# Performance work log

Measured on AMD Instinct MI355X. Metric: run time of the kernel, lower is better.

Reference implementation:

```python
import jax, jax.numpy as jnp
import numpy as np
import math

BATCH = 32
F_IN, F_OUT = 16, 32
B_IN, B_OUT = 16, 8
N_SPEC = B_OUT * (4 * B_OUT ** 2 - 1) // 3  # sum_{l<b_out} (2l+1)^2 = 680
ALPHAS = [2.0 * np.pi * a / 6.0 for a in range(6)]
GAMMAS = [2.0 * np.pi * c / 4.0 for c in range(4)]
GRID = [(al, np.pi / 16.0, ga) for al in ALPHAS for ga in GAMMAS]  # 24 (alpha, beta, gamma) points
SCALING = 1.0 / math.sqrt(len(GRID) * F_IN * B_OUT ** 3 / B_IN ** 3)


def _wigner_d(l, beta):
    """Wigner small-d matrix d^l_{m'm}(beta), centered order m',m=-l..l, quantum/Condon-Shortley."""
    lg = math.lgamma
    cb, sb = math.cos(beta / 2.0), math.sin(beta / 2.0)
    d = np.zeros((2 * l + 1, 2 * l + 1))
    for i, mp in enumerate(range(-l, l + 1)):
        for j, m in enumerate(range(-l, l + 1)):
            pref = 0.5 * (lg(l + mp + 1) + lg(l - mp + 1) + lg(l + m + 1) + lg(l - m + 1))
            tot = 0.0
            for s in range(max(0, m - mp), min(l + m, l - mp) + 1):
                den = lg(l + m - s + 1) + lg(s + 1) + lg(mp - m + s + 1) + lg(l - mp - s + 1)
                tot += ((-1.0) ** (mp - m + s) * math.exp(pref - den)
                        * cb ** (2 * l + m - mp - 2 * s) * sb ** (mp - m + 2 * s))
            d[i, j] = tot
    return d


def _quad_weights(b):
    """SOFT quadrature weights at beta_j = pi(2j+1)/(4b); 1/(2b)^2 absorbs the unnormalized 2D FFT."""
    k = np.arange(b)
    j = np.arange(2 * b)
    w = (2.0 / b) * np.sin(np.pi * (2 * j + 1) / (4.0 * b)) * (
        np.sin(np.pi * np.outer(2 * j + 1, 2 * k + 1) / (4.0 * b)) / (2 * k + 1)).sum(axis=1)
    return w / (2 * b) ** 2


def _setup_tables():
    betas_in = np.pi * (2 * np.arange(2 * B_IN) + 1) / (4.0 * B_IN)
    betas_out = np.pi * (2 * np.arange(2 * B_OUT) + 1) / (4.0 * B_OUT)
    w = _quad_weights(B_IN)
    wig_fwd = np.stack([np.concatenate([w[j] * _wigner_d(l, b).ravel() for l in range(B_OUT)])
                        for j, b in enumerate(betas_in)])          # [2*B_IN, N_SPEC]
    wig_inv = np.stack([np.concatenate([(2 * l + 1) * _wigner_d(l, b).ravel() for l in range(B_OUT)])
                        for b in betas_out])                       # [2*B_OUT, N_SPEC]
    F = np.zeros((len(GRID), N_SPEC), dtype=np.complex128)
    for p, (al, be, ga) in enumerate(GRID):
        blocks = []
        for l in range(B_OUT):
            m = np.arange(-l, l + 1)
            D = np.exp(-1j * m[:, None] * al) * _wigner_d(l, be) * np.exp(-1j * m[None, :] * ga)
            blocks.append(np.conj(D).ravel())
        F[p] = np.concatenate(blocks)
    return (wig_fwd.astype(np.float32), wig_inv.astype(np.float32),
            F.real.astype(np.float32), F.imag.astype(np.float32))


def _freq_idx(l, n):
    # packed frequencies -l..-1,0..l with wraparound into an FFT axis of length n
    return np.r_[np.arange(n - l, n), np.arange(l + 1)] if l > 0 else np.arange(1)


def _forward(x, kernel, bias, wigner_fwd, wigner_inv, ft_re, ft_im):
    xf = jnp.fft.fft2(x)  # FFT over (alpha, gamma): [B, Fin, 2b_in, 2b_in, 2b_in] complex64
    # SO3_fft_real: weighted Wigner-d contraction over beta, per degree l
    xhat = []
    for l in range(B_OUT):
        idx = _freq_idx(l, 2 * B_IN)
        xx = xf[:, :, :, idx[:, None], idx[None, :]]  # [B, Fin, beta, 2l+1, 2l+1]
        s0 = l * (4 * l * l - 1) // 3
        wl = wigner_fwd[:, s0:s0 + (2 * l + 1) ** 2].reshape(2 * B_IN, 2 * l + 1, 2 * l + 1)
        xhat.append(jnp.einsum('bmn,zfbmn->mnzf', wl, xx))  # [2l+1, 2l+1, B, Fin]
    # so3_rft of the scaled kernel on the grid: yhat [N_SPEC, Fin, Fout]
    Fc = ft_re + 1j * ft_im  # [P, N_SPEC]
    yhat = jnp.einsum('iop,ps->sio', (kernel * SCALING).astype(jnp.complex64), Fc)
    # so3_mm: per-degree z^l = x^l (y^l)^H, then inverse SO3 FFT
    B = x.shape[0]
    ff = jnp.zeros((B, F_OUT, 2 * B_OUT, 2 * B_OUT, 2 * B_OUT), dtype=xf.dtype)
    for l in range(B_OUT):
        s0 = l * (4 * l * l - 1) // 3
        yl = yhat[s0:s0 + (2 * l + 1) ** 2].reshape(2 * l + 1, 2 * l + 1, F_IN, F_OUT)
        zl = jnp.einsum('mkzf,nkfg->mnzg', xhat[l], jnp.conj(yl))  # [2l+1, 2l+1, B, Fout]
        wl = wigner_inv[:, s0:s0 + (2 * l + 1) ** 2].reshape(2 * B_OUT, 2 * l + 1, 2 * l + 1)
        o = jnp.einsum('mnzg,bmn->zgbmn', zl, wl)  # [B, Fout, beta_out, 2l+1, 2l+1]
        idx = _freq_idx(l, 2 * B_OUT)
        ff = ff.at[:, :, :, idx[:, None], idx[None, :]].add(o)
    out = jnp.real(jnp.fft.ifft2(ff)) * float((2 * B_OUT) ** 2)  # undo ifft 1/N^2, keep real part
    return out + bias


def setup_inputs():
    key = jax.random.key(0)
    k1, k2 = jax.random.split(key)
    x = jax.random.normal(k1, (BATCH, F_IN, 2 * B_IN, 2 * B_IN, 2 * B_IN), dtype=jnp.float32)
    kernel = jax.random.uniform(k2, (F_IN, F_OUT, len(GRID)), minval=-1.0, maxval=1.0, dtype=jnp.float32)
    bias = jnp.zeros((1, F_OUT, 1, 1, 1), jnp.float32)
    wf, wi, fre, fim = _setup_tables()
    return {"x": x, "kernel": kernel, "bias": bias,
            "wigner_fwd": jnp.asarray(wf), "wigner_inv": jnp.asarray(wi),
            "ft_re": jnp.asarray(fre), "ft_im": jnp.asarray(fim)}


def reference(x, kernel, bias, wigner_fwd, wigner_inv, ft_re, ft_im):
    return _forward(x, kernel, bias, wigner_fwd, wigner_inv, ft_re, ft_im)
```

## Files before the change

### kernel.cpp

```cpp
#include <hip/hip_runtime.h>
#include <math.h>


#define NS 680
#define NR 372
#define NP 24
#define NW 15
#define SLB 4
#define SCALING 0.14433756729740643f

__device__ __constant__ int c_s0[9] = {0, 1, 10, 35, 84, 165, 286, 455, 680};
__device__ __constant__ int c_o[9]  = {0, 1, 7, 22, 50, 95, 161, 252, 372};

__device__ __constant__ float2 TW32[32] = {
    { 1.0000000000f,  0.0000000000f}, { 0.9807852804f, -0.1950903220f},
    { 0.9238795325f, -0.3826834324f}, { 0.8314696123f, -0.5555702330f},
    { 0.7071067812f, -0.7071067812f}, { 0.5555702330f, -0.8314696123f},
    { 0.3826834324f, -0.9238795325f}, { 0.1950903220f, -0.9807852804f},
    { 0.0000000000f, -1.0000000000f}, {-0.1950903220f, -0.9807852804f},
    {-0.3826834324f, -0.9238795325f}, {-0.5555702330f, -0.8314696123f},
    {-0.7071067812f, -0.7071067812f}, {-0.8314696123f, -0.5555702330f},
    {-0.9238795325f, -0.3826834324f}, {-0.9807852804f, -0.1950903220f},
    {-1.0000000000f,  0.0000000000f}, {-0.9807852804f,  0.1950903220f},
    {-0.9238795325f,  0.3826834324f}, {-0.8314696123f,  0.5555702330f},
    {-0.7071067812f,  0.7071067812f}, {-0.5555702330f,  0.8314696123f},
    {-0.3826834324f,  0.9238795325f}, {-0.1950903220f,  0.9807852804f},
    { 0.0000000000f,  1.0000000000f}, { 0.1950903220f,  0.9807852804f},
    { 0.3826834324f,  0.9238795325f}, { 0.5555702330f,  0.8314696123f},
    { 0.7071067812f,  0.7071067812f}, { 0.8314696123f,  0.5555702330f},
    { 0.9238795325f,  0.3826834324f}, { 0.9807852804f,  0.1950903220f}};

__device__ __constant__ float2 TW16P[16] = {
    { 1.0000000000f,  0.0000000000f}, { 0.9238795325f,  0.3826834324f},
    { 0.7071067812f,  0.7071067812f}, { 0.3826834324f,  0.9238795325f},
    { 0.0000000000f,  1.0000000000f}, {-0.3826834324f,  0.9238795325f},
    {-0.7071067812f,  0.7071067812f}, {-0.9238795325f,  0.3826834324f},
    {-1.0000000000f,  0.0000000000f}, {-0.9238795325f, -0.3826834324f},
    {-0.7071067812f, -0.7071067812f}, {-0.3826834324f, -0.9238795325f},
    { 0.0000000000f, -1.0000000000f}, { 0.3826834324f, -0.9238795325f},
    { 0.7071067812f, -0.7071067812f}, { 0.9238795325f, -0.3826834324f}};

__global__ __launch_bounds__(256) void A12(const float* __restrict__ x,
                                           float2* __restrict__ xf2) {
    __shared__ __align__(16) float  sx[SLB * 1152];
    __shared__ __align__(16) float2 st[SLB][8][34];
    __shared__ float2 tw[32];
    int blk = blockIdx.x;
    int tid = threadIdx.x;
    if (tid < 32) tw[tid] = TW32[tid];
    {
        const float4* xs = (const float4*)(x + (size_t)blk * (SLB * 1024));
#pragma unroll
        for (int q = 0; q < SLB; q++) {
            int idx = q * 256 + tid;
            float4 v4 = xs[idx];
            int sl = idx >> 8, w = idx & 255;
            *(float4*)&sx[sl * 1152 + (w >> 3) * 36 + (w & 7) * 4] = v4;
        }
    }
    __syncthreads();
    {
        int u = tid >> 3, n = tid & 7;
        float sgn = (n & 1) ? -1.f : 1.f;
        float2 t8[8];
#pragma unroll
        for (int c = 0; c < 8; c++) t8[c] = tw[(n * c) & 31];
        float2 fa1 = tw[(8 * n) & 31];
#pragma unroll
        for (int sl = 0; sl < SLB; sl++) {
            const float* row = &sx[sl * 1152 + u * 36];
            float4 x0 = *(float4*)&row[0],  x1 = *(float4*)&row[4];
            float4 x2 = *(float4*)&row[8],  x3 = *(float4*)&row[12];
            float4 x4 = *(float4*)&row[16], x5 = *(float4*)&row[20];
            float4 x6 = *(float4*)&row[24], x7 = *(float4*)&row[28];
            float y0  = fmaf(sgn, x4.x, x0.x), y1  = fmaf(sgn, x4.y, x0.y);
            float y2  = fmaf(sgn, x4.z, x0.z), y3  = fmaf(sgn, x4.w, x0.w);
            float y4  = fmaf(sgn, x5.x, x1.x), y5  = fmaf(sgn, x5.y, x1.y);
            float y6  = fmaf(sgn, x5.z, x1.z), y7  = fmaf(sgn, x5.w, x1.w);
            float y8  = fmaf(sgn, x6.x, x2.x), y9  = fmaf(sgn, x6.y, x2.y);
            float y10 = fmaf(sgn, x6.z, x2.z), y11 = fmaf(sgn, x6.w, x2.w);
            float y12 = fmaf(sgn, x7.x, x3.x), y13 = fmaf(sgn, x7.y, x3.y);
            float y14 = fmaf(sgn, x7.z, x3.z), y15 = fmaf(sgn, x7.w, x3.w);
            float p0r = y0 * t8[0].x + y1 * t8[1].x + y2 * t8[2].x + y3 * t8[3].x
                      + y4 * t8[4].x + y5 * t8[5].x + y6 * t8[6].x + y7 * t8[7].x;
            float p0i = y0 * t8[0].y + y1 * t8[1].y + y2 * t8[2].y + y3 * t8[3].y
                      + y4 * t8[4].y + y5 * t8[5].y + y6 * t8[6].y + y7 * t8[7].y;
            float p1r = y8 * t8[0].x + y9 * t8[1].x + y10 * t8[2].x + y11 * t8[3].x
                      + y12 * t8[4].x + y13 * t8[5].x + y14 * t8[6].x + y15 * t8[7].x;
            float p1i = y8 * t8[0].y + y9 * t8[1].y + y10 * t8[2].y + y11 * t8[3].y
                      + y12 * t8[4].y + y13 * t8[5].y + y14 * t8[6].y + y15 * t8[7].y;
            float re = p0r + fa1.x * p1r - fa1.y * p1i;
            float im = p0i + fa1.x * p1i + fa1.y * p1r;
            st[sl][n][u] = make_float2(re, im);
        }
    }
    __syncthreads();
    {
        int sl = tid >> 6, m = (tid >> 3) & 7, jj = tid & 7;
        float2 t8[8], fa[4];
#pragma unroll
        for (int c = 0; c < 8; c++) t8[c] = tw[(m * c) & 31];
        fa[0] = make_float2(1.f, 0.f);
#pragma unroll
        for (int a = 1; a < 4; a++) fa[a] = tw[(8 * m * a) & 31];
        float reP = 0.f, imP = 0.f, reN = 0.f, imN = 0.f;
#pragma unroll
        for (int a = 0; a < 4; a++) {
            const float4* spt = (const float4*)&st[sl][jj][a * 8];
            float4 r0 = spt[0], r1 = spt[1], r2 = spt[2], r3 = spt[3];
            float A = r0.x * t8[0].x + r0.z * t8[1].x + r1.x * t8[2].x + r1.z * t8[3].x
                    + r2.x * t8[4].x + r2.z * t8[5].x + r3.x * t8[6].x + r3.z * t8[7].x;
            float B = r0.y * t8[0].y + r0.w * t8[1].y + r1.y * t8[2].y + r1.w * t8[3].y
                    + r2.y * t8[4].y + r2.w * t8[5].y + r3.y * t8[6].y + r3.w * t8[7].y;
            float C = r0.x * t8[0].y + r0.z * t8[1].y + r1.x * t8[2].y + r1.z * t8[3].y
                    + r2.x * t8[4].y + r2.z * t8[5].y + r3.x * t8[6].y + r3.z * t8[7].y;
            float D = r0.y * t8[0].x + r0.w * t8[1].x + r1.y * t8[2].x + r1.w * t8[3].x
                    + r2.y * t8[4].x + r2.w * t8[5].x + r3.y * t8[6].x + r3.w * t8[7].x;
            float prP = A - B, piP = C + D;
            float prN = A + B, piN = C - D;
            reP += fa[a].x * prP - fa[a].y * piP;
            imP += fa[a].x * piP + fa[a].y * prP;
            reN += fa[a].x * prN - fa[a].y * piN;
            imN += fa[a].x * piN + fa[a].y * prN;
        }
        int slice = blk * SLB + sl;
        float2* ob = xf2 + (size_t)slice * 120 + m * 15;
        ob[7 + jj] = make_float2(reP, imP);
        if (jj) ob[7 - jj] = make_float2(reN, imN);
    }
}

__global__ void kP(const float* __restrict__ kern, const float* __restrict__ fre,
                   const float* __restrict__ fim, const float* __restrict__ wf,
                   const float* __restrict__ wi, float2* __restrict__ yhat,
                   float* __restrict__ wfT, float* __restrict__ wiTd) {
    int idx = blockIdx.x * blockDim.x + threadIdx.x;
    if (idx < NS * 512) {
        int s = idx >> 9, fg = idx & 511;
        float re = 0.f, im = 0.f;
        for (int p = 0; p < NP; p++) {
            float kv = kern[fg * NP + p];
            re += kv * fre[p * NS + s];
            im += kv * fim[p * NS + s];
        }
        yhat[(size_t)s * 512 + fg] = make_float2(re * SCALING, im * SCALING);
        return;
    }
    int j = idx - NS * 512;
    if (j < NR * 32) {
        int sp = j >> 5, b = j & 31;
        int l = 0;
#pragma unroll
        for (int t = 1; t < 8; t++) if (sp >= c_o[t]) l = t;
        int K = 2 * l + 1, r = sp - c_o[l];
        int m = r / K, jn = r - m * K;
        int sf = c_s0[l] + (m + l) * K + jn;
        wfT[sp * 32 + b] = wf[b * NS + sf];
        return;
    }
    int k = j - NR * 32;
    if (k >= 16384) return;
    int ni = k & 15, mm = (k >> 4) & 7, b8 = (k >> 7) & 7;
    int l = (k >> 10) & 7, bh = k >> 13;
    int nn = ni - 7;
    float v = 0.f;
    if (ni < 15 && mm <= l && nn >= -l && nn <= l) {
        int K = 2 * l + 1;
        v = wi[(bh * 8 + b8) * NS + c_s0[l] + (mm + l) * K + (nn + l)];
    }
    wiTd[k] = v;
}

__global__ __launch_bounds__(256) void A3(const float2* __restrict__ xf2,
                                          const float* __restrict__ wfT,
                                          float2* __restrict__ xhat) {
    __shared__ float2 sxf[32 * 120];
    int zf = blockIdx.x >> 1, sh = blockIdx.x & 1;
    int tid = threadIdx.x;
    for (int t = tid; t < 32 * 120; t += 256)
        sxf[t] = xf2[(size_t)zf * (32 * 120) + t];
    __syncthreads();
    if (tid < 186) {
        int sp = sh * 186 + tid;
        int l = 0;
#pragma unroll
        for (int t = 1; t < 8; t++) if (sp >= c_o[t]) l = t;
        int K = 2 * l + 1, r = sp - c_o[l];
        int m = r / K, jn = r - m * K;
        int cell = m * 15 + (jn - l + 7);
        const float4* wp = (const float4*)(wfT + sp * 32);
        const float2* xp = sxf + cell;
        float re = 0.f, im = 0.f;
#pragma unroll
        for (int q = 0; q < 8; q++) {
            float4 w4 = wp[q];
            float2 v0 = xp[(q * 4 + 0) * 120];
            float2 v1 = xp[(q * 4 + 1) * 120];
            float2 v2 = xp[(q * 4 + 2) * 120];
            float2 v3 = xp[(q * 4 + 3) * 120];
            re += w4.x * v0.x + w4.y * v1.x + w4.z * v2.x + w4.w * v3.x;
            im += w4.x * v0.y + w4.y * v1.y + w4.z * v2.y + w4.w * v3.y;
        }
        xhat[(size_t)sp * 512 + zf] = make_float2(re, im);
    }
}

__global__ __launch_bounds__(256) void kD(const float2* __restrict__ xhat,
                                          const float2* __restrict__ yhat,
                                          float2* __restrict__ zbuf) {
    __shared__ float2 Xs[4][16][18];
    __shared__ float2 Ys[4][16][34];
    int sp = 371 - (blockIdx.x >> 1);
    int zh = blockIdx.x & 1;
    int l = 0;
#pragma unroll
    for (int t = 1; t < 8; t++) if (sp >= c_o[t]) l = t;
    int K = 2 * l + 1, r = sp - c_o[l];
    int m = r / K, jn = r - m * K;
    int sX0 = c_o[l] + m * K;
    int sY0 = c_s0[l] + jn * K;
    int tid = threadIdx.x;
    int zl = tid >> 4;
    int g0 = (tid & 15) * 2;
    float2 acc0 = make_float2(0.f, 0.f), acc1 = make_float2(0.f, 0.f);
    int nchunks = (K + 3) >> 2;
    for (int chunk = 0; chunk < nchunks; ++chunk) {
#pragma unroll
        for (int kw = 0; kw < 4; kw++) {
            int k = chunk * 4 + kw;
            if (k < K)
                Xs[kw][tid & 15][tid >> 4] =
                    xhat[(size_t)(sX0 + k) * 512 + (zh * 16 + (tid >> 4)) * 16 + (tid & 15)];
        }
#pragma unroll
        for (int it = 0; it < 8; it++) {
            int kw = it >> 1;
            int fg = (it & 1) * 256 + tid;
            int k = chunk * 4 + kw;
            if (k < K)
                Ys[kw][fg >> 5][fg & 31] = yhat[(size_t)(sY0 + k) * 512 + fg];
        }
        __syncthreads();
#pragma unroll
        for (int kw = 0; kw < 4; kw++) {
            int k = chunk * 4 + kw;
            if (k < K) {
#pragma unroll
                for (int f = 0; f < 16; f++) {
                    float2 xv  = Xs[kw][f][zl];
                    float2 yv0 = Ys[kw][f][g0];
                    float2 yv1 = Ys[kw][f][g0 + 1];
                    acc0.x += xv.x * yv0.x + xv.y * yv0.y;
                    acc0.y += xv.y * yv0.x - xv.x * yv0.y;
                    acc1.x += xv.x * yv1.x + xv.y * yv1.y;
                    acc1.y += xv.y * yv1.x - xv.x * yv1.y;
                }
            }
        }
        __syncthreads();
    }
    int z0 = zh * 16 + zl;
    zbuf[(size_t)sp * 1024 + z0 * 32 + g0]     = acc0;
    zbuf[(size_t)sp * 1024 + z0 * 32 + g0 + 1] = acc1;
}

__global__ __launch_bounds__(256) void kE3(const float2* __restrict__ zbuf,
                                           const float* __restrict__ wiTd,
                                           const float* __restrict__ bias,
                                           float* __restrict__ out) {
    __shared__ float2 szp[384];
    __shared__ float2 g1[8][129];
    __shared__ float2 tw[16];
    int zg = blockIdx.x >> 1, bh = blockIdx.x & 1;
    int g = zg & 31;
    int tid = threadIdx.x;
    if (tid < 16) tw[tid] = TW16P[tid];
    if (tid < 8)   szp[tid] = make_float2(0.f, 0.f);
    if (tid >= 252) szp[tid + 128] = make_float2(0.f, 0.f);
    for (int t = tid; t < NR; t += 256) szp[8 + t] = zbuf[(size_t)t * 1024 + zg];
    __syncthreads();
    if (tid < 128) {
        int b8 = tid & 7, mm = (tid >> 3) & 7, vh = tid >> 6;
        const int co[8] = {0, 1, 7, 22, 50, 95, 161, 252};
        float2 ff[15];
#pragma unroll
        for (int n = 0; n < 15; n++) ff[n] = make_float2(0.f, 0.f);
#pragma unroll
        for (int l = 0; l < 8; l++) {
            const float4* wl = (const float4*)(wiTd + ((((bh * 8 + l) * 8 + b8) * 8 + mm) << 4));
            float4 w0 = wl[0], w1 = wl[1], w2 = wl[2], w3 = wl[3];
            float wreg[16] = {w0.x, w0.y, w0.z, w0.w, w1.x, w1.y, w1.z, w1.w,
                              w2.x, w2.y, w2.z, w2.w, w3.x, w3.y, w3.z, w3.w};
            int sp = 1 + co[l] + mm * (2 * l + 1) + l;
#pragma unroll
            for (int ni = 0; ni < 15; ni++) {
                float w = wreg[ni];
                float2 v = szp[sp + ni];
                ff[ni].x += w * v.x; ff[ni].y += w * v.y;
            }
        }
#pragma unroll
        for (int j = 0; j < 8; j++) {
            int v = vh * 8 + j;
            float re = 0.f, im = 0.f;
#pragma unroll
            for (int n = 0; n < 15; n++) {
                float2 c = tw[((n - 7) * v) & 15];
                float2 a = ff[n];
                re += a.x * c.x - a.y * c.y;
                im += a.x * c.y + a.y * c.x;
            }
            g1[b8][mm * 16 + v] = make_float2(re, im);
        }
    }
    __syncthreads();
    {
        int b8 = tid & 7, u = (tid >> 3) & 15, vh = tid >> 7;
        int b = bh * 8 + b8;
        int v0 = vh * 8;
        float o[8];
#pragma unroll
        for (int j = 0; j < 8; j++) o[j] = g1[b8][v0 + j].x;
#pragma unroll
        for (int m = 1; m < 8; m++) {
            float2 c = tw[(m * u) & 15];
#pragma unroll
            for (int j = 0; j < 8; j++) {
                float2 a = g1[b8][m * 16 + v0 + j];
                o[j] += 2.f * (a.x * c.x - a.y * c.y);
            }
        }
        float bv = bias[g];
        float* ob = out + ((size_t)zg * 16 + b) * 256 + u * 16 + v0;
        *(float4*)&ob[0] = make_float4(o[0] + bv, o[1] + bv, o[2] + bv, o[3] + bv);
        *(float4*)&ob[4] = make_float4(o[4] + bv, o[5] + bv, o[6] + bv, o[7] + bv);
    }
}

extern "C" void kernel_launch(void* const* d_in, const int* in_sizes, int n_in,
                              void* d_out, int out_size, void* d_ws, size_t ws_size,
                              hipStream_t stream) {
    const float* x    = (const float*)d_in[0];
    const float* kern = (const float*)d_in[1];
    const float* bias = (const float*)d_in[2];
    const float* wf   = (const float*)d_in[3];
    const float* wi   = (const float*)d_in[4];
    const float* fre  = (const float*)d_in[5];
    const float* fim  = (const float*)d_in[6];
    float* out = (float*)d_out;

    char* ws = (char*)d_ws;
    float2* xf2  = (float2*)ws;
    float2* xhat = (float2*)(ws + 15728640);
    float2* yhat = (float2*)(ws + 17252352);
    float2* zbuf = (float2*)(ws + 20037632);
    float*  wfT  = (float*)(ws + 23085056);
    float*  wiTd = (float*)(ws + 23132672);

    A12<<<4096, 256, 0, stream>>>(x, xf2);
    kP<<<1471, 256, 0, stream>>>(kern, fre, fim, wf, wi, yhat, wfT, wiTd);
    A3<<<1024, 256, 0, stream>>>(xf2, wfT, xhat);
    kD<<<744, 256, 0, stream>>>(xhat, yhat, zbuf);
    kE3<<<2048, 256, 0, stream>>>(zbuf, wiTd, bias, out);
}
```

Before: 92.66 us.

## Transpose zbuf via new kernel for coalesced kE3 loads; pad g1 shared array

Adds a tiled shared-memory transpose kernel that rewrites zbuf from [sp][zg] to [zg][sp] layout. kE3 can then read its 372 spectral coefficients contiguously instead of with a 1024-element stride. The g1 shared buffer is also re-padded (stride 17 per m, 139 per b8) to reduce bank conflicts. The cost is an extra kernel launch plus roughly 6 MB of extra global traffic through the transpose.

```diff
diff --git a/kernel.cpp b/kernel.cpp
--- a/kernel.cpp
+++ b/kernel.cpp
@@ -264,12 +264,33 @@
     zbuf[(size_t)sp * 1024 + z0 * 32 + g0 + 1] = acc1;
 }
 
-__global__ __launch_bounds__(256) void kE3(const float2* __restrict__ zbuf,
+__global__ __launch_bounds__(256) void kX(const float2* __restrict__ zbuf,
+                                          float2* __restrict__ zbufT) {
+    __shared__ float2 st[32][33];
+    int spT = blockIdx.x % 12, zgT = blockIdx.x / 12;
+    int sp0 = spT * 32, zg0 = zgT * 32;
+    int tid = threadIdx.x;
+#pragma unroll
+    for (int r = 0; r < 4; r++) {
+        int idx = r * 256 + tid;
+        int i = idx >> 5, j = idx & 31;
+        if (sp0 + i < NR) st[i][j] = zbuf[(size_t)(sp0 + i) * 1024 + zg0 + j];
+    }
+    __syncthreads();
+#pragma unroll
+    for (int r = 0; r < 4; r++) {
+        int idx = r * 256 + tid;
+        int i = idx >> 5, j = idx & 31;
+        if (sp0 + j < NR) zbufT[(size_t)(zg0 + i) * NR + sp0 + j] = st[j][i];
+    }
+}
+
+__global__ __launch_bounds__(256) void kE3(const float2* __restrict__ zbufT,
                                            const float* __restrict__ wiTd,
                                            const float* __restrict__ bias,
                                            float* __restrict__ out) {
     __shared__ float2 szp[384];
-    __shared__ float2 g1[8][129];
+    __shared__ float2 g1[8 * 139];
     __shared__ float2 tw[16];
     int zg = blockIdx.x >> 1, bh = blockIdx.x & 1;
     int g = zg & 31;
@@ -277,7 +298,7 @@
     if (tid < 16) tw[tid] = TW16P[tid];
     if (tid < 8)   szp[tid] = make_float2(0.f, 0.f);
     if (tid >= 252) szp[tid + 128] = make_float2(0.f, 0.f);
-    for (int t = tid; t < NR; t += 256) szp[8 + t] = zbuf[(size_t)t * 1024 + zg];
+    for (int t = tid; t < NR; t += 256) szp[8 + t] = zbufT[(size_t)zg * NR + t];
     __syncthreads();
     if (tid < 128) {
         int b8 = tid & 7, mm = (tid >> 3) & 7, vh = tid >> 6;
@@ -310,7 +331,7 @@
                 re += a.x * c.x - a.y * c.y;
                 im += a.x * c.y + a.y * c.x;
             }
-            g1[b8][mm * 16 + v] = make_float2(re, im);
+            g1[b8 * 139 + mm * 17 + v] = make_float2(re, im);
         }
     }
     __syncthreads();
@@ -320,13 +341,13 @@
         int v0 = vh * 8;
         float o[8];
 #pragma unroll
-        for (int j = 0; j < 8; j++) o[j] = g1[b8][v0 + j].x;
+        for (int j = 0; j < 8; j++) o[j] = g1[b8 * 139 + v0 + j].x;
 #pragma unroll
         for (int m = 1; m < 8; m++) {
             float2 c = tw[(m * u) & 15];
 #pragma unroll
             for (int j = 0; j < 8; j++) {
-                float2 a = g1[b8][m * 16 + v0 + j];
+                float2 a = g1[b8 * 139 + m * 17 + v0 + j];
                 o[j] += 2.f * (a.x * c.x - a.y * c.y);
             }
         }
@@ -350,16 +371,18 @@
     float* out = (float*)d_out;
 
     char* ws = (char*)d_ws;
-    float2* xf2  = (float2*)ws;
-    float2* xhat = (float2*)(ws + 15728640);
-    float2* yhat = (float2*)(ws + 17252352);
-    float2* zbuf = (float2*)(ws + 20037632);
-    float*  wfT  = (float*)(ws + 23085056);
-    float*  wiTd = (float*)(ws + 23132672);
+    float2* xf2   = (float2*)ws;
+    float2* xhat  = (float2*)(ws + 15728640);
+    float2* yhat  = (float2*)(ws + 17252352);
+    float2* zbuf  = (float2*)(ws + 20037632);
+    float*  wfT   = (float*)(ws + 23085056);
+    float*  wiTd  = (float*)(ws + 23132672);
+    float2* zbufT = (float2*)(ws + 23198208);
 
     A12<<<4096, 256, 0, stream>>>(x, xf2);
     kP<<<1471, 256, 0, stream>>>(kern, fre, fim, wf, wi, yhat, wfT, wiTd);
     A3<<<1024, 256, 0, stream>>>(xf2, wfT, xhat);
     kD<<<744, 256, 0, stream>>>(xhat, yhat, zbuf);
-    kE3<<<2048, 256, 0, stream>>>(zbuf, wiTd, bias, out);
-}
+    kX<<<384, 256, 0, stream>>>(zbuf, zbufT);
+    kE3<<<2048, 256, 0, stream>>>(zbufT, wiTd, bias, out);
+}
```

New measurement: 94.13 us. Within noise of the previous version (+1.6%).

## Merge block halves in A3 and kE, transpose zbuf for contiguous reads

Applied to the files above, without the earlier changes.

A3 now uses one block per zf whose threads cover all 372 spectral entries, so the 30KB shared staging of xf2 is loaded once per zf rather than twice. kD writes z in transposed layout [z,g][sp], so the final kernel reads its 372 coefficients contiguously instead of with a 1024-element stride. kE4 processes all 16 beta rows per block with a padded shared buffer, halving the block count and the redundant loads. The trade-off is fewer blocks, more work per thread, and strided scattered writes in kD.

```diff
diff --git a/kernel.cpp b/kernel.cpp
--- a/kernel.cpp
+++ b/kernel.cpp
@@ -175,13 +175,15 @@
                                           const float* __restrict__ wfT,
                                           float2* __restrict__ xhat) {
     __shared__ float2 sxf[32 * 120];
-    int zf = blockIdx.x >> 1, sh = blockIdx.x & 1;
+    int zf = blockIdx.x;
     int tid = threadIdx.x;
     for (int t = tid; t < 32 * 120; t += 256)
         sxf[t] = xf2[(size_t)zf * (32 * 120) + t];
     __syncthreads();
-    if (tid < 186) {
-        int sp = sh * 186 + tid;
+#pragma unroll
+    for (int q = 0; q < 2; q++) {
+        if (q == 1 && tid >= 116) break;
+        int sp = tid + q * 256;
         int l = 0;
 #pragma unroll
         for (int t = 1; t < 8; t++) if (sp >= c_o[t]) l = t;
@@ -192,12 +194,12 @@
         const float2* xp = sxf + cell;
         float re = 0.f, im = 0.f;
 #pragma unroll
-        for (int q = 0; q < 8; q++) {
-            float4 w4 = wp[q];
-            float2 v0 = xp[(q * 4 + 0) * 120];
-            float2 v1 = xp[(q * 4 + 1) * 120];
-            float2 v2 = xp[(q * 4 + 2) * 120];
-            float2 v3 = xp[(q * 4 + 3) * 120];
+        for (int qq = 0; qq < 8; qq++) {
+            float4 w4 = wp[qq];
+            float2 v0 = xp[(qq * 4 + 0) * 120];
+            float2 v1 = xp[(qq * 4 + 1) * 120];
+            float2 v2 = xp[(qq * 4 + 2) * 120];
+            float2 v3 = xp[(qq * 4 + 3) * 120];
             re += w4.x * v0.x + w4.y * v1.x + w4.z * v2.x + w4.w * v3.x;
             im += w4.x * v0.y + w4.y * v1.y + w4.z * v2.y + w4.w * v3.y;
         }
@@ -207,7 +209,7 @@
 
 __global__ __launch_bounds__(256) void kD(const float2* __restrict__ xhat,
                                           const float2* __restrict__ yhat,
-                                          float2* __restrict__ zbuf) {
+                                          float2* __restrict__ zbufT) {
     __shared__ float2 Xs[4][16][18];
     __shared__ float2 Ys[4][16][34];
     int sp = 371 - (blockIdx.x >> 1);
@@ -260,27 +262,28 @@
         __syncthreads();
     }
     int z0 = zh * 16 + zl;
-    zbuf[(size_t)sp * 1024 + z0 * 32 + g0]     = acc0;
-    zbuf[(size_t)sp * 1024 + z0 * 32 + g0 + 1] = acc1;
-}
-
-__global__ __launch_bounds__(256) void kE3(const float2* __restrict__ zbuf,
+    zbufT[(size_t)(z0 * 32 + g0) * NR + sp]     = acc0;
+    zbufT[(size_t)(z0 * 32 + g0 + 1) * NR + sp] = acc1;
+}
+
+__global__ __launch_bounds__(256) void kE4(const float2* __restrict__ zbufT,
                                            const float* __restrict__ wiTd,
                                            const float* __restrict__ bias,
                                            float* __restrict__ out) {
     __shared__ float2 szp[384];
-    __shared__ float2 g1[8][129];
+    __shared__ float2 g1[16 * 139];
     __shared__ float2 tw[16];
-    int zg = blockIdx.x >> 1, bh = blockIdx.x & 1;
+    int zg = blockIdx.x;
     int g = zg & 31;
     int tid = threadIdx.x;
     if (tid < 16) tw[tid] = TW16P[tid];
-    if (tid < 8)   szp[tid] = make_float2(0.f, 0.f);
+    if (tid < 8)    szp[tid] = make_float2(0.f, 0.f);
     if (tid >= 252) szp[tid + 128] = make_float2(0.f, 0.f);
-    for (int t = tid; t < NR; t += 256) szp[8 + t] = zbuf[(size_t)t * 1024 + zg];
-    __syncthreads();
-    if (tid < 128) {
-        int b8 = tid & 7, mm = (tid >> 3) & 7, vh = tid >> 6;
+    for (int t = tid; t < NR; t += 256) szp[8 + t] = zbufT[(size_t)zg * NR + t];
+    __syncthreads();
+    {
+        int b = tid & 15, mm = (tid >> 4) & 7, vh = tid >> 7;
+        int bh = b >> 3, b8 = b & 7;
         const int co[8] = {0, 1, 7, 22, 50, 95, 161, 252};
         float2 ff[15];
 #pragma unroll
@@ -310,30 +313,29 @@
                 re += a.x * c.x - a.y * c.y;
                 im += a.x * c.y + a.y * c.x;
             }
-            g1[b8][mm * 16 + v] = make_float2(re, im);
-        }
-    }
-    __syncthreads();
-    {
-        int b8 = tid & 7, u = (tid >> 3) & 15, vh = tid >> 7;
-        int b = bh * 8 + b8;
-        int v0 = vh * 8;
-        float o[8];
-#pragma unroll
-        for (int j = 0; j < 8; j++) o[j] = g1[b8][v0 + j].x;
+            g1[b * 139 + mm * 17 + v] = make_float2(re, im);
+        }
+    }
+    __syncthreads();
+    {
+        int b = tid & 15, u = tid >> 4;
+        float o[16];
+#pragma unroll
+        for (int j = 0; j < 16; j++) o[j] = g1[b * 139 + j].x;
 #pragma unroll
         for (int m = 1; m < 8; m++) {
             float2 c = tw[(m * u) & 15];
 #pragma unroll
-            for (int j = 0; j < 8; j++) {
-                float2 a = g1[b8][m * 16 + v0 + j];
+            for (int j = 0; j < 16; j++) {
+                float2 a = g1[b * 139 + m * 17 + j];
                 o[j] += 2.f * (a.x * c.x - a.y * c.y);
             }
         }
         float bv = bias[g];
-        float* ob = out + ((size_t)zg * 16 + b) * 256 + u * 16 + v0;
-        *(float4*)&ob[0] = make_float4(o[0] + bv, o[1] + bv, o[2] + bv, o[3] + bv);
-        *(float4*)&ob[4] = make_float4(o[4] + bv, o[5] + bv, o[6] + bv, o[7] + bv);
+        float* ob = out + ((size_t)zg * 16 + b) * 256 + u * 16;
+#pragma unroll
+        for (int j = 0; j < 16; j += 4)
+            *(float4*)&ob[j] = make_float4(o[j] + bv, o[j + 1] + bv, o[j + 2] + bv, o[j + 3] + bv);
     }
 }
 
@@ -350,16 +352,16 @@
     float* out = (float*)d_out;
 
     char* ws = (char*)d_ws;
-    float2* xf2  = (float2*)ws;
-    float2* xhat = (float2*)(ws + 15728640);
-    float2* yhat = (float2*)(ws + 17252352);
-    float2* zbuf = (float2*)(ws + 20037632);
-    float*  wfT  = (float*)(ws + 23085056);
-    float*  wiTd = (float*)(ws + 23132672);
+    float2* xf2   = (float2*)ws;
+    float2* xhat  = (float2*)(ws + 15728640);
+    float2* yhat  = (float2*)(ws + 17252352);
+    float2* zbufT = (float2*)(ws + 20037632);
+    float*  wfT   = (float*)(ws + 23085056);
+    float*  wiTd  = (float*)(ws + 23132672);
 
     A12<<<4096, 256, 0, stream>>>(x, xf2);
     kP<<<1471, 256, 0, stream>>>(kern, fre, fim, wf, wi, yhat, wfT, wiTd);
-    A3<<<1024, 256, 0, stream>>>(xf2, wfT, xhat);
-    kD<<<744, 256, 0, stream>>>(xhat, yhat, zbuf);
-    kE3<<<2048, 256, 0, stream>>>(zbuf, wiTd, bias, out);
-}
+    A3<<<512, 256, 0, stream>>>(xf2, wfT, xhat);
+    kD<<<744, 256, 0, stream>>>(xhat, yhat, zbufT);
+    kE4<<<1024, 256, 0, stream>>>(zbufT, wiTd, bias, out);
+}
```

Result: faster. 87.82 us (-5.2%).
